# Kernel tuning notes

Hardware: AMD Instinct MI355X
Metric: run time of the kernel (lower is better)

Reference implementation:

```python
import jax, jax.numpy as jnp
import numpy as np

D_IN = 1024
D_OUT = 1024
N_HEADS = 16
HEAD_DIM = D_OUT // N_HEADS
B = 2
S = 2048


def setup_inputs() -> dict:
    key = jax.random.key(0)
    ks = jax.random.split(key, 6)
    scale = 0.02
    x = jax.random.normal(ks[0], (B, S, D_IN), dtype=jnp.float32)
    # torch nn.Linear stores weight as [out, in]; y = x @ W.T + b
    Wq = jax.random.normal(ks[1], (D_OUT, D_IN), dtype=jnp.float32) * scale
    Wk = jax.random.normal(ks[2], (D_OUT, D_IN), dtype=jnp.float32) * scale
    Wv = jax.random.normal(ks[3], (D_OUT, D_IN), dtype=jnp.float32) * scale
    Wo = jax.random.normal(ks[4], (D_OUT, D_OUT), dtype=jnp.float32) * scale
    bo = jax.random.normal(ks[5], (D_OUT,), dtype=jnp.float32) * scale
    return {"x": x, "Wq": Wq, "Wk": Wk, "Wv": Wv, "Wo": Wo, "bo": bo}


def reference(x, Wq, Wk, Wv, Wo, bo):
    b, n, _ = x.shape
    # projections (no qkv bias)
    q = jnp.einsum('bnd,ed->bne', x, Wq).reshape(b, n, N_HEADS, HEAD_DIM).transpose(0, 2, 1, 3)
    k = jnp.einsum('bnd,ed->bne', x, Wk).reshape(b, n, N_HEADS, HEAD_DIM).transpose(0, 2, 1, 3)
    v = jnp.einsum('bnd,ed->bne', x, Wv).reshape(b, n, N_HEADS, HEAD_DIM).transpose(0, 2, 1, 3)
    # scores [b, h, s, s]
    scores = jnp.einsum('bhqd,bhkd->bhqk', q, k) / jnp.sqrt(jnp.float32(HEAD_DIM))
    causal = jnp.tril(jnp.ones((n, n), dtype=bool))
    scores = jnp.where(causal, scores, -jnp.inf)
    attn = jax.nn.softmax(scores, axis=-1)  # dropout p=0 -> identity
    ctx = jnp.einsum('bhqk,bhkd->bhqd', attn, v)
    ctx = ctx.transpose(0, 2, 1, 3).reshape(b, n, D_OUT)
    out = jnp.einsum('bnd,ed->bne', ctx, Wo) + bo
    return out
```

## Files before the change

### kernel.cpp

```cpp
#include <hip/hip_runtime.h>

typedef unsigned short u16;
typedef unsigned int u32;
typedef short bf16x8 __attribute__((ext_vector_type(8)));
typedef short bf16x4 __attribute__((ext_vector_type(4)));
typedef float f32x4 __attribute__((ext_vector_type(4)));
typedef u32 u32x2 __attribute__((ext_vector_type(2)));

#define LOG2E 1.4426950408889634f
#define QSCALE (0.125f * LOG2E)

__device__ __forceinline__ u16 f2b(float f) {
  u32 u = __builtin_bit_cast(u32, f);
  u32 r = (u + 0x7FFFu + ((u >> 16) & 1u)) >> 16;
  return (u16)r;
}

__device__ __forceinline__ bf16x8 cvt8(const float* p) {
  const f32x4 a = *(const f32x4*)p;
  const f32x4 b = *(const f32x4*)(p + 4);
  bf16x8 r = { (short)f2b(a[0]), (short)f2b(a[1]), (short)f2b(a[2]),
               (short)f2b(a[3]), (short)f2b(b[0]), (short)f2b(b[1]),
               (short)f2b(b[2]), (short)f2b(b[3]) };
  return r;
}

__device__ __forceinline__ void gl_lds16(const u16* g, u16* l) {
  __builtin_amdgcn_global_load_lds(
      (const __attribute__((address_space(1))) u32*)(const void*)g,
      (__attribute__((address_space(3))) u32*)(void*)l, 16, 0, 0);
}

__global__ __launch_bounds__(256) void convert_qw_kernel(
    const float* __restrict__ x, const float* __restrict__ wq,
    const float* __restrict__ wk, const float* __restrict__ wv,
    u16* __restrict__ xb, u16* __restrict__ wb) {
  const int i = blockIdx.x * 256 + threadIdx.x;
  if (i >= 917504) return;
  const float* src;
  u16* dst;
  size_t off;
  if (i < 524288) {
    src = x; dst = xb; off = (size_t)i * 8;
  } else {
    const int j = i - 524288;
    const int mat = j >> 17, r = j & 131071;
    src = (mat == 0) ? wq : ((mat == 1) ? wk : wv);
    dst = wb + (size_t)mat * 1048576u;
    off = (size_t)r * 8;
  }
  *(bf16x8*)(dst + off) = cvt8(src + off);
}

__device__ __forceinline__ void gemm_core3(const u16* A, const u16* W,
                                           int m0, int n0, int tid,
                                           u16* As, u16* Bs,
                                           f32x4 (&acc)[4][4]) {
  const int lane = tid & 63, wave = tid >> 6;
  const int wr = wave >> 1, wc = wave & 1;
  const int l15 = lane & 15, quad = lane >> 4;

  const int srow = wave * 16 + (lane >> 2);
  const int csrc =
      (((lane & 3) ^ ((lane >> 2) & 3) ^ ((lane >> 4) & 3)) << 3);
  const u16* ga = A + (size_t)(m0 + srow) * 1024 + csrc;
  const u16* gw = W + (size_t)(n0 + srow) * 1024 + csrc;
  const int lo = wave * 16 * 32;

  const int rswz = (l15 & 3) ^ ((l15 >> 2) & 3);
  const int aoff = (wr * 64 + l15) * 32 + ((quad ^ rswz) << 3);
  const int boff = (wc * 64 + l15) * 32 + ((quad ^ rswz) << 3);

  auto stage = [&](int k0, int db) {
    u16* la = As + db * 4096 + lo;
    u16* lb = Bs + db * 4096 + lo;
    gl_lds16(ga + k0, la);
    gl_lds16(ga + k0 + (size_t)64 * 1024, la + 64 * 32);
    gl_lds16(gw + k0, lb);
    gl_lds16(gw + k0 + (size_t)64 * 1024, lb + 64 * 32);
  };

  stage(0, 0);
  __syncthreads();
  int db = 0;
  for (int k0 = 0; k0 < 1024; k0 += 32) {
    if (k0 + 32 < 1024) stage(k0 + 32, db ^ 1);
    const u16* ar = As + db * 4096 + aoff;
    const u16* br = Bs + db * 4096 + boff;
    bf16x8 af[4], bfr[4];
#pragma unroll
    for (int i = 0; i < 4; ++i) af[i] = *(const bf16x8*)(ar + i * 16 * 32);
#pragma unroll
    for (int i = 0; i < 4; ++i) bfr[i] = *(const bf16x8*)(br + i * 16 * 32);
#pragma unroll
    for (int mt = 0; mt < 4; ++mt)
#pragma unroll
      for (int nt = 0; nt < 4; ++nt)
        acc[mt][nt] = __builtin_amdgcn_mfma_f32_16x16x32_bf16(
            af[mt], bfr[nt], acc[mt][nt], 0, 0, 0);
    __syncthreads();
    db ^= 1;
  }
}

__device__ __forceinline__ void gemm_core_out(const u16* A, const float* Wf,
                                              int m0, int n0, int klo, int tid,
                                              u16* As, u16* Bs,
                                              f32x4 (&acc)[4][4]) {
  const int lane = tid & 63, wave = tid >> 6;
  const int wr = wave >> 1, wc = wave & 1;
  const int l15 = lane & 15, quad = lane >> 4;

  const int srow = wave * 16 + (lane >> 2);
  const int csrc =
      (((lane & 3) ^ ((lane >> 2) & 3) ^ ((lane >> 4) & 3)) << 3);
  const u16* ga = A + (size_t)(m0 + srow) * 1024 + csrc;
  const float* gw = Wf + (size_t)(n0 + srow) * 1024 + csrc;
  const int lo = wave * 512;

  const int rswz = (l15 & 3) ^ ((l15 >> 2) & 3);
  const int aoff = (wr * 64 + l15) * 32 + ((quad ^ rswz) << 3);
  const int boff = (wc * 64 + l15) * 32 + ((quad ^ rswz) << 3);

  auto stageA = [&](int k0, int db) {
    u16* la = As + db * 4096 + lo;
    gl_lds16(ga + k0, la);
    gl_lds16(ga + k0 + (size_t)64 * 1024, la + 64 * 32);
  };
  auto loadW = [&](int k0, f32x4 (&w)[4]) {
    w[0] = *(const f32x4*)(gw + k0);
    w[1] = *(const f32x4*)(gw + k0 + 4);
    w[2] = *(const f32x4*)(gw + k0 + 65536);
    w[3] = *(const f32x4*)(gw + k0 + 65540);
  };
  auto writeW = [&](f32x4 (&w)[4], int db) {
    u16* lb = Bs + db * 4096 + lo + lane * 8;
    bf16x8 w0 = { (short)f2b(w[0][0]), (short)f2b(w[0][1]), (short)f2b(w[0][2]),
                  (short)f2b(w[0][3]), (short)f2b(w[1][0]), (short)f2b(w[1][1]),
                  (short)f2b(w[1][2]), (short)f2b(w[1][3]) };
    bf16x8 w1 = { (short)f2b(w[2][0]), (short)f2b(w[2][1]), (short)f2b(w[2][2]),
                  (short)f2b(w[2][3]), (short)f2b(w[3][0]), (short)f2b(w[3][1]),
                  (short)f2b(w[3][2]), (short)f2b(w[3][3]) };
    *(bf16x8*)lb = w0;
    *(bf16x8*)(lb + 2048) = w1;
  };

  f32x4 wreg[4];
  stageA(klo, 0);
  loadW(klo, wreg);
  writeW(wreg, 0);
  __syncthreads();
  int db = 0;
  const int kend = klo + 512;
  for (int k0 = klo; k0 < kend; k0 += 32) {
    const bool more = (k0 + 32 < kend);
    f32x4 wnext[4];
    if (more) {
      stageA(k0 + 32, db ^ 1);
      loadW(k0 + 32, wnext);
    }
    const u16* ar = As + db * 4096 + aoff;
    const u16* br = Bs + db * 4096 + boff;
    bf16x8 af[4], bfr[4];
#pragma unroll
    for (int i = 0; i < 4; ++i) af[i] = *(const bf16x8*)(ar + i * 16 * 32);
#pragma unroll
    for (int i = 0; i < 4; ++i) bfr[i] = *(const bf16x8*)(br + i * 16 * 32);
#pragma unroll
    for (int mt = 0; mt < 4; ++mt)
#pragma unroll
      for (int nt = 0; nt < 4; ++nt)
        acc[mt][nt] = __builtin_amdgcn_mfma_f32_16x16x32_bf16(
            af[mt], bfr[nt], acc[mt][nt], 0, 0, 0);
    if (more) writeW(wnext, db ^ 1);
    __syncthreads();
    db ^= 1;
  }
}

__global__ __launch_bounds__(256, 3) void gemm_qkv_kernel(
    const u16* __restrict__ xb, const u16* __restrict__ wb,
    u16* __restrict__ qo, u16* __restrict__ ko, u16* __restrict__ vt) {
  __shared__ __align__(16) u16 As[2 * 128 * 32];
  __shared__ __align__(16) u16 Bs[2 * 128 * 32];
  const int tid = threadIdx.x;
  const int m0 = blockIdx.x * 128;
  const int mat = blockIdx.y >> 3;
  const int n0 = (blockIdx.y & 7) * 128;
  const u16* W = wb + (size_t)mat * 1048576u;

  f32x4 acc[4][4] = {};
  gemm_core3(xb, W, m0, n0, tid, As, Bs, acc);

  const int lane = tid & 63, wave = tid >> 6;
  const int wr = wave >> 1, wc = wave & 1;
  const int l15 = lane & 15, quad = lane >> 4;

  if (mat < 2) {
    u16* out = (mat == 0) ? qo : ko;
    const float sc = (mat == 0) ? QSCALE : 1.0f;
#pragma unroll
    for (int mt = 0; mt < 4; ++mt) {
      const int gr = m0 + wr * 64 + mt * 16 + quad * 4;
#pragma unroll
      for (int nt = 0; nt < 4; ++nt) {
        const int gc = n0 + wc * 64 + nt * 16 + l15;
#pragma unroll
        for (int r = 0; r < 4; ++r)
          out[(size_t)(gr + r) * 1024 + gc] = f2b(acc[mt][nt][r] * sc);
      }
    }
  } else {
#pragma unroll
    for (int mt = 0; mt < 4; ++mt) {
      const int gr = m0 + wr * 64 + mt * 16 + quad * 4;
      const int b = gr >> 11;
      const int s = gr & 2047;
#pragma unroll
      for (int nt = 0; nt < 4; ++nt) {
        const int gc = n0 + wc * 64 + nt * 16 + l15;
        bf16x4 pk = { (short)f2b(acc[mt][nt][0]), (short)f2b(acc[mt][nt][1]),
                      (short)f2b(acc[mt][nt][2]), (short)f2b(acc[mt][nt][3]) };
        *(bf16x4*)&vt[(size_t)(b * 1024 + gc) * 2048 + s] = pk;
      }
    }
  }
}

__global__ __launch_bounds__(256, 2) void gemm_out_kernel(
    const u16* __restrict__ ctx, const float* __restrict__ wo,
    float* __restrict__ part, float* __restrict__ out) {
  __shared__ __align__(16) u16 As[2 * 128 * 32];
  __shared__ __align__(16) u16 Bs[2 * 128 * 32];
  const int tid = threadIdx.x;
  const int m0 = blockIdx.x * 128;
  const int n0 = blockIdx.y * 128;
  const int klo = blockIdx.z * 512;

  f32x4 acc[4][4] = {};
  gemm_core_out(ctx, wo, m0, n0, klo, tid, As, Bs, acc);

  float* dst = (blockIdx.z == 0) ? part : out;
  const int lane = tid & 63, wave = tid >> 6;
  const int wr = wave >> 1, wc = wave & 1;
  const int l15 = lane & 15, quad = lane >> 4;
#pragma unroll
  for (int nt = 0; nt < 4; ++nt) {
    const int gc = n0 + wc * 64 + nt * 16 + l15;
#pragma unroll
    for (int mt = 0; mt < 4; ++mt) {
      const int gr = m0 + wr * 64 + mt * 16 + quad * 4;
#pragma unroll
      for (int r = 0; r < 4; ++r)
        dst[(size_t)(gr + r) * 1024 + gc] = acc[mt][nt][r];
    }
  }
}

__global__ __launch_bounds__(256) void merge_out_kernel(
    float* __restrict__ out, const float* __restrict__ part,
    const float* __restrict__ bo) {
  const int i = (blockIdx.x * 256 + threadIdx.x) * 4;
  const f32x4 a = *(const f32x4*)(out + i);
  const f32x4 p = *(const f32x4*)(part + i);
  const f32x4 bv = *(const f32x4*)(bo + (i & 1023));
  f32x4 r = { a[0] + p[0] + bv[0], a[1] + p[1] + bv[1],
              a[2] + p[2] + bv[2], a[3] + p[3] + bv[3] };
  *(f32x4*)(out + i) = r;
}

__global__ __launch_bounds__(256, 4) void flash_kernel(
    const u16* q, const u16* __restrict__ k,
    const u16* __restrict__ vt, u16* ctx) {
  __shared__ __align__(16) u16 Ks[2][4096];
  __shared__ __align__(16) u16 Vs[2][4096];
  __shared__ __align__(16) u16 plds_all[4][1024];

  const int tid = threadIdx.x;
  const int wave = tid >> 6, lane = tid & 63;
  const int l15 = lane & 15, quad = lane >> 4;

  const int g = blockIdx.x;
  const int xcd = g & 7;
  const int s = g >> 3;
  const int bh_local = s >> 5;
  const int c = s & 31;
  const int qv = (bh_local & 1) ? (31 - c) : c;
  const int q0b = qv * 64;
  const int ntiles = qv + 1;
  const int bh = xcd + 8 * bh_local;
  const int b = bh >> 4, h = bh & 15;
  const int m = q0b + wave * 16 + l15;

  const u16* qrow = q + ((size_t)(b * 2048 + m) * 1024 + h * 64);
  const bf16x8 qf0 = *(const bf16x8*)(qrow + quad * 8);
  const bf16x8 qf1 = *(const bf16x8*)(qrow + 32 + quad * 8);

  const int sr = wave * 16 + (lane >> 3);
  const int csrc = (((lane & 7) ^ ((lane >> 3) & 7)) << 3);
  const u16* kg = k + (size_t)(b * 2048) * 1024 + h * 64;
  const u16* vg = vt + (size_t)(b * 1024 + h * 64) * 2048;
  u16* plds = plds_all[wave];
  const int swz = (l15 & 7);

  f32x4 o[4] = {};
  float m_run = -INFINITY, l_lane = 0.0f;

#pragma unroll
  for (int i = 0; i < 2; ++i) {
    const int r = sr + i * 8;
    gl_lds16(kg + (size_t)r * 1024 + csrc, &Ks[0][wave * 1024 + i * 512]);
    gl_lds16(vg + (size_t)r * 2048 + csrc, &Vs[0][wave * 1024 + i * 512]);
  }
  __syncthreads();

  int buf = 0;
  for (int t = 0; t < ntiles; ++t) {
    const int n0 = t * 64;
    if (t + 1 < ntiles) {
      const int n1 = n0 + 64;
      const int nb = buf ^ 1;
#pragma unroll
      for (int i = 0; i < 2; ++i) {
        const int r = sr + i * 8;
        gl_lds16(kg + (size_t)(n1 + r) * 1024 + csrc,
                 &Ks[nb][wave * 1024 + i * 512]);
        gl_lds16(vg + (size_t)r * 2048 + n1 + csrc,
                 &Vs[nb][wave * 1024 + i * 512]);
      }
    }

    f32x4 st[4];
#pragma unroll
    for (int s4 = 0; s4 < 4; ++s4) {
      const u16* kr = &Ks[buf][(s4 * 16 + l15) * 64];
      const bf16x8 kf0 = *(const bf16x8*)(kr + ((quad ^ swz) << 3));
      const bf16x8 kf1 = *(const bf16x8*)(kr + (((4 | quad) ^ swz) << 3));
      f32x4 a = {};
      a = __builtin_amdgcn_mfma_f32_16x16x32_bf16(kf0, qf0, a, 0, 0, 0);
      a = __builtin_amdgcn_mfma_f32_16x16x32_bf16(kf1, qf1, a, 0, 0, 0);
      st[s4] = a;
    }

    float s[16];
#pragma unroll
    for (int s4 = 0; s4 < 4; ++s4)
#pragma unroll
      for (int r = 0; r < 4; ++r) s[s4 * 4 + r] = st[s4][r];
    if (t == ntiles - 1) {
#pragma unroll
      for (int s4 = 0; s4 < 4; ++s4)
#pragma unroll
        for (int r = 0; r < 4; ++r) {
          const int kv = n0 + s4 * 16 + quad * 4 + r;
          if (kv > m) s[s4 * 4 + r] = -INFINITY;
        }
    }
    float t8[8], t4[4];
#pragma unroll
    for (int i = 0; i < 8; ++i) t8[i] = fmaxf(s[i], s[i + 8]);
#pragma unroll
    for (int i = 0; i < 4; ++i) t4[i] = fmaxf(t8[i], t8[i + 4]);
    float mx = fmaxf(fmaxf(t4[0], t4[1]), fmaxf(t4[2], t4[3]));
    mx = fmaxf(mx, __shfl_xor(mx, 16));
    mx = fmaxf(mx, __shfl_xor(mx, 32));

    float mbase;
    if (__all(mx <= m_run + 8.0f)) {
      mbase = m_run;
    } else {
      mbase = fmaxf(m_run, mx);
      const float alpha = exp2f(m_run - mbase);
      l_lane *= alpha;
#pragma unroll
      for (int dt = 0; dt < 4; ++dt) o[dt] *= alpha;
      m_run = mbase;
    }

    float p[16];
#pragma unroll
    for (int i = 0; i < 16; ++i) p[i] = exp2f(s[i] - mbase);
    float u8[8], u4[4];
#pragma unroll
    for (int i = 0; i < 8; ++i) u8[i] = p[i] + p[i + 8];
#pragma unroll
    for (int i = 0; i < 4; ++i) u4[i] = u8[i] + u8[i + 4];
    l_lane += (u4[0] + u4[1]) + (u4[2] + u4[3]);

#pragma unroll
    for (int s4 = 0; s4 < 4; ++s4) {
      u32 c0, c1;
      asm("v_cvt_pk_bf16_f32 %0, %1, %2"
          : "=v"(c0) : "v"(p[s4 * 4 + 0]), "v"(p[s4 * 4 + 1]));
      asm("v_cvt_pk_bf16_f32 %0, %1, %2"
          : "=v"(c1) : "v"(p[s4 * 4 + 2]), "v"(p[s4 * 4 + 3]));
      const int wchunk = ((s4 * 2 + (quad >> 1)) ^ swz) << 3;
      u32x2 w = { c0, c1 };
      *(u32x2*)&plds[l15 * 64 + wchunk + ((quad & 1) << 2)] = w;
    }
    asm volatile("s_waitcnt lgkmcnt(0)" ::: "memory");

#pragma unroll
    for (int ks = 0; ks < 2; ++ks) {
      const bf16x8 pf =
          *(const bf16x8*)&plds[l15 * 64 + (((ks * 4 + quad) ^ swz) << 3)];
#pragma unroll
      for (int dt = 0; dt < 4; ++dt) {
        const u16* vr = &Vs[buf][(dt * 16 + l15) * 64];
        const bf16x8 vf =
            *(const bf16x8*)(vr + ((((ks << 2) | quad) ^ swz) << 3));
        o[dt] = __builtin_amdgcn_mfma_f32_16x16x32_bf16(vf, pf, o[dt], 0, 0, 0);
      }
    }

    __syncthreads();
    buf ^= 1;
  }

  float l = l_lane;
  l += __shfl_xor(l, 16);
  l += __shfl_xor(l, 32);
  const float inv = 1.0f / l;
  u16* crow = ctx + ((size_t)(b * 2048 + m) * 1024 + h * 64);
#pragma unroll
  for (int dt = 0; dt < 4; ++dt) {
    bf16x4 ov = { (short)f2b(o[dt][0] * inv), (short)f2b(o[dt][1] * inv),
                  (short)f2b(o[dt][2] * inv), (short)f2b(o[dt][3] * inv) };
    *(bf16x4*)&crow[dt * 16 + quad * 4] = ov;
  }
}

extern "C" void kernel_launch(void* const* d_in, const int* in_sizes, int n_in,
                              void* d_out, int out_size, void* d_ws,
                              size_t ws_size, hipStream_t stream) {
  const float* x  = (const float*)d_in[0];
  const float* wq = (const float*)d_in[1];
  const float* wk = (const float*)d_in[2];
  const float* wv = (const float*)d_in[3];
  const float* wo = (const float*)d_in[4];
  const float* bo = (const float*)d_in[5];
  float* out = (float*)d_out;

  u16* qb = (u16*)d_ws;
  u16* kb = qb + 4194304u;
  u16* vt = kb + 4194304u;
  u16* ctx = qb;
  float* part = (float*)kb;

  u16* xb = (u16*)d_out;
  u16* wb = xb + 4194304u;

  convert_qw_kernel<<<3584, 256, 0, stream>>>(x, wq, wk, wv, xb, wb);
  gemm_qkv_kernel<<<dim3(32, 24), 256, 0, stream>>>(xb, wb, qb, kb, vt);
  flash_kernel<<<1024, 256, 0, stream>>>(qb, kb, vt, ctx);
  gemm_out_kernel<<<dim3(32, 8, 2), 256, 0, stream>>>(ctx, wo, part, out);
  merge_out_kernel<<<4096, 256, 0, stream>>>(out, part, bo);
}
```

Before: 196.6 us.

## Replace split-K output GEMM and merge with 128x64-tile GEMM fusing bias

```diff
diff --git a/kernel.cpp b/kernel.cpp
--- a/kernel.cpp
+++ b/kernel.cpp
@@ -103,82 +103,7 @@
   }
 }
 
-__device__ __forceinline__ void gemm_core_out(const u16* A, const float* Wf,
-                                              int m0, int n0, int klo, int tid,
-                                              u16* As, u16* Bs,
-                                              f32x4 (&acc)[4][4]) {
-  const int lane = tid & 63, wave = tid >> 6;
-  const int wr = wave >> 1, wc = wave & 1;
-  const int l15 = lane & 15, quad = lane >> 4;
-
-  const int srow = wave * 16 + (lane >> 2);
-  const int csrc =
-      (((lane & 3) ^ ((lane >> 2) & 3) ^ ((lane >> 4) & 3)) << 3);
-  const u16* ga = A + (size_t)(m0 + srow) * 1024 + csrc;
-  const float* gw = Wf + (size_t)(n0 + srow) * 1024 + csrc;
-  const int lo = wave * 512;
-
-  const int rswz = (l15 & 3) ^ ((l15 >> 2) & 3);
-  const int aoff = (wr * 64 + l15) * 32 + ((quad ^ rswz) << 3);
-  const int boff = (wc * 64 + l15) * 32 + ((quad ^ rswz) << 3);
-
-  auto stageA = [&](int k0, int db) {
-    u16* la = As + db * 4096 + lo;
-    gl_lds16(ga + k0, la);
-    gl_lds16(ga + k0 + (size_t)64 * 1024, la + 64 * 32);
-  };
-  auto loadW = [&](int k0, f32x4 (&w)[4]) {
-    w[0] = *(const f32x4*)(gw + k0);
-    w[1] = *(const f32x4*)(gw + k0 + 4);
-    w[2] = *(const f32x4*)(gw + k0 + 65536);
-    w[3] = *(const f32x4*)(gw + k0 + 65540);
-  };
-  auto writeW = [&](f32x4 (&w)[4], int db) {
-    u16* lb = Bs + db * 4096 + lo + lane * 8;
-    bf16x8 w0 = { (short)f2b(w[0][0]), (short)f2b(w[0][1]), (short)f2b(w[0][2]),
-                  (short)f2b(w[0][3]), (short)f2b(w[1][0]), (short)f2b(w[1][1]),
-                  (short)f2b(w[1][2]), (short)f2b(w[1][3]) };
-    bf16x8 w1 = { (short)f2b(w[2][0]), (short)f2b(w[2][1]), (short)f2b(w[2][2]),
-                  (short)f2b(w[2][3]), (short)f2b(w[3][0]), (short)f2b(w[3][1]),
-                  (short)f2b(w[3][2]), (short)f2b(w[3][3]) };
-    *(bf16x8*)lb = w0;
-    *(bf16x8*)(lb + 2048) = w1;
-  };
-
-  f32x4 wreg[4];
-  stageA(klo, 0);
-  loadW(klo, wreg);
-  writeW(wreg, 0);
-  __syncthreads();
-  int db = 0;
-  const int kend = klo + 512;
-  for (int k0 = klo; k0 < kend; k0 += 32) {
-    const bool more = (k0 + 32 < kend);
-    f32x4 wnext[4];
-    if (more) {
-      stageA(k0 + 32, db ^ 1);
-      loadW(k0 + 32, wnext);
-    }
-    const u16* ar = As + db * 4096 + aoff;
-    const u16* br = Bs + db * 4096 + boff;
-    bf16x8 af[4], bfr[4];
-#pragma unroll
-    for (int i = 0; i < 4; ++i) af[i] = *(const bf16x8*)(ar + i * 16 * 32);
-#pragma unroll
-    for (int i = 0; i < 4; ++i) bfr[i] = *(const bf16x8*)(br + i * 16 * 32);
-#pragma unroll
-    for (int mt = 0; mt < 4; ++mt)
-#pragma unroll
-      for (int nt = 0; nt < 4; ++nt)
-        acc[mt][nt] = __builtin_amdgcn_mfma_f32_16x16x32_bf16(
-            af[mt], bfr[nt], acc[mt][nt], 0, 0, 0);
-    if (more) writeW(wnext, db ^ 1);
-    __syncthreads();
-    db ^= 1;
-  }
-}
-
-__global__ __launch_bounds__(256, 3) void gemm_qkv_kernel(
+__global__ __launch_bounds__(256, 4) void gemm_qkv_kernel(
     const u16* __restrict__ xb, const u16* __restrict__ wb,
     u16* __restrict__ qo, u16* __restrict__ ko, u16* __restrict__ vt) {
   __shared__ __align__(16) u16 As[2 * 128 * 32];
@@ -227,46 +152,95 @@
   }
 }
 
-__global__ __launch_bounds__(256, 2) void gemm_out_kernel(
+__global__ __launch_bounds__(256, 4) void gemm_out_kernel(
     const u16* __restrict__ ctx, const float* __restrict__ wo,
-    float* __restrict__ part, float* __restrict__ out) {
+    const float* __restrict__ bo, float* __restrict__ out) {
   __shared__ __align__(16) u16 As[2 * 128 * 32];
-  __shared__ __align__(16) u16 Bs[2 * 128 * 32];
+  __shared__ __align__(16) u16 Bs[2 * 64 * 32];
   const int tid = threadIdx.x;
   const int m0 = blockIdx.x * 128;
-  const int n0 = blockIdx.y * 128;
-  const int klo = blockIdx.z * 512;
-
-  f32x4 acc[4][4] = {};
-  gemm_core_out(ctx, wo, m0, n0, klo, tid, As, Bs, acc);
-
-  float* dst = (blockIdx.z == 0) ? part : out;
+  const int n0 = blockIdx.y * 64;
+
   const int lane = tid & 63, wave = tid >> 6;
   const int wr = wave >> 1, wc = wave & 1;
   const int l15 = lane & 15, quad = lane >> 4;
-#pragma unroll
-  for (int nt = 0; nt < 4; ++nt) {
-    const int gc = n0 + wc * 64 + nt * 16 + l15;
+
+  const int srow = wave * 16 + (lane >> 2);
+  const int csrc =
+      (((lane & 3) ^ ((lane >> 2) & 3) ^ ((lane >> 4) & 3)) << 3);
+  const u16* ga = ctx + (size_t)(m0 + srow) * 1024 + csrc;
+  const int lo = wave * 512;
+
+  const int rb = tid >> 2;
+  const int csrcB =
+      (((tid & 3) ^ ((tid >> 2) & 3) ^ ((tid >> 4) & 3)) << 3);
+  const float* gw = wo + (size_t)(n0 + rb) * 1024 + csrcB;
+
+  const int rswz = (l15 & 3) ^ ((l15 >> 2) & 3);
+  const int aoff = (wr * 64 + l15) * 32 + ((quad ^ rswz) << 3);
+  const int boff = (wc * 32 + l15) * 32 + ((quad ^ rswz) << 3);
+
+  auto stageA = [&](int k0, int db) {
+    u16* la = As + db * 4096 + lo;
+    gl_lds16(ga + k0, la);
+    gl_lds16(ga + k0 + (size_t)64 * 1024, la + 64 * 32);
+  };
+  auto loadW = [&](int k0, f32x4 (&w)[2]) {
+    w[0] = *(const f32x4*)(gw + k0);
+    w[1] = *(const f32x4*)(gw + k0 + 4);
+  };
+  auto writeW = [&](f32x4 (&w)[2], int db) {
+    u16* lb = Bs + db * 2048 + tid * 8;
+    bf16x8 p = { (short)f2b(w[0][0]), (short)f2b(w[0][1]), (short)f2b(w[0][2]),
+                 (short)f2b(w[0][3]), (short)f2b(w[1][0]), (short)f2b(w[1][1]),
+                 (short)f2b(w[1][2]), (short)f2b(w[1][3]) };
+    *(bf16x8*)lb = p;
+  };
+
+  f32x4 acc[4][2] = {};
+  f32x4 wreg[2];
+  stageA(0, 0);
+  loadW(0, wreg);
+  writeW(wreg, 0);
+  __syncthreads();
+  int db = 0;
+  for (int k0 = 0; k0 < 1024; k0 += 32) {
+    const bool more = (k0 + 32 < 1024);
+    f32x4 wnext[2];
+    if (more) {
+      stageA(k0 + 32, db ^ 1);
+      loadW(k0 + 32, wnext);
+    }
+    const u16* ar = As + db * 4096 + aoff;
+    const u16* br = Bs + db * 2048 + boff;
+    bf16x8 af[4], bfr[2];
+#pragma unroll
+    for (int i = 0; i < 4; ++i) af[i] = *(const bf16x8*)(ar + i * 16 * 32);
+#pragma unroll
+    for (int i = 0; i < 2; ++i) bfr[i] = *(const bf16x8*)(br + i * 16 * 32);
+#pragma unroll
+    for (int mt = 0; mt < 4; ++mt)
+#pragma unroll
+      for (int nt = 0; nt < 2; ++nt)
+        acc[mt][nt] = __builtin_amdgcn_mfma_f32_16x16x32_bf16(
+            af[mt], bfr[nt], acc[mt][nt], 0, 0, 0);
+    if (more) writeW(wnext, db ^ 1);
+    __syncthreads();
+    db ^= 1;
+  }
+
+#pragma unroll
+  for (int nt = 0; nt < 2; ++nt) {
+    const int gc = n0 + wc * 32 + nt * 16 + l15;
+    const float bv = bo[gc];
 #pragma unroll
     for (int mt = 0; mt < 4; ++mt) {
       const int gr = m0 + wr * 64 + mt * 16 + quad * 4;
 #pragma unroll
       for (int r = 0; r < 4; ++r)
-        dst[(size_t)(gr + r) * 1024 + gc] = acc[mt][nt][r];
-    }
-  }
-}
-
-__global__ __launch_bounds__(256) void merge_out_kernel(
-    float* __restrict__ out, const float* __restrict__ part,
-    const float* __restrict__ bo) {
-  const int i = (blockIdx.x * 256 + threadIdx.x) * 4;
-  const f32x4 a = *(const f32x4*)(out + i);
-  const f32x4 p = *(const f32x4*)(part + i);
-  const f32x4 bv = *(const f32x4*)(bo + (i & 1023));
-  f32x4 r = { a[0] + p[0] + bv[0], a[1] + p[1] + bv[1],
-              a[2] + p[2] + bv[2], a[3] + p[3] + bv[3] };
-  *(f32x4*)(out + i) = r;
+        out[(size_t)(gr + r) * 1024 + gc] = acc[mt][nt][r] + bv;
+    }
+  }
 }
 
 __global__ __launch_bounds__(256, 4) void flash_kernel(
@@ -445,7 +419,6 @@
   u16* kb = qb + 4194304u;
   u16* vt = kb + 4194304u;
   u16* ctx = qb;
-  float* part = (float*)kb;
 
   u16* xb = (u16*)d_out;
   u16* wb = xb + 4194304u;
@@ -453,6 +426,5 @@
   convert_qw_kernel<<<3584, 256, 0, stream>>>(x, wq, wk, wv, xb, wb);
   gemm_qkv_kernel<<<dim3(32, 24), 256, 0, stream>>>(xb, wb, qb, kb, vt);
   flash_kernel<<<1024, 256, 0, stream>>>(qb, kb, vt, ctx);
-  gemm_out_kernel<<<dim3(32, 8, 2), 256, 0, stream>>>(ctx, wo, part, out);
-  merge_out_kernel<<<4096, 256, 0, stream>>>(out, part, bo);
-}
+  gemm_out_kernel<<<dim3(32, 16), 256, 0, stream>>>(ctx, wo, bo, out);
+}
```

Result: no change. 195.4 us (-0.6%).
